# Kernel tuning notes

Measured on AMD Instinct MI355X. Metric: run time of the kernel, lower is better.

The kernel has to match this reference:

```python
import jax, jax.numpy as jnp
import numpy as np

B, N, DIM, H, DH, M, ROT = 2, 2048, 1024, 16, 64, 16, 32


def setup_inputs() -> dict:
    key = jax.random.key(0)
    ks = jax.random.split(key, 10)
    x = jax.random.normal(ks[0], (B, N, DIM), dtype=jnp.float32)
    # standard rotary frequency table, duplicated halves: [1,1,N,ROT]
    inv_freq = 1.0 / (10000.0 ** (jnp.arange(0, ROT, 2, dtype=jnp.float32) / ROT))
    t = jnp.arange(N, dtype=jnp.float32)
    fr = jnp.einsum('i,j->ij', t, inv_freq)
    rotary_pos_emb = jnp.concatenate([fr, fr], axis=-1)[None, None]
    s = 0.02
    Wq = jax.random.normal(ks[1], (H * DH, DIM), dtype=jnp.float32) * s
    Wk = jax.random.normal(ks[2], (H * DH, DIM), dtype=jnp.float32) * s
    Wv = jax.random.normal(ks[3], (H * DH, DIM), dtype=jnp.float32) * s
    mem_k = jax.random.normal(ks[4], (H, M, DH), dtype=jnp.float32)
    mem_v = jax.random.normal(ks[5], (H, M, DH), dtype=jnp.float32)
    pre_proj = jax.random.normal(ks[6], (H, H), dtype=jnp.float32)
    post_proj = jax.random.normal(ks[7], (H, H), dtype=jnp.float32)
    Wo = jax.random.normal(ks[8], (DIM, H * DH), dtype=jnp.float32) * s
    bo = jnp.zeros((DIM,), dtype=jnp.float32)
    return {'x': x, 'rotary_pos_emb': rotary_pos_emb, 'Wq': Wq, 'Wk': Wk, 'Wv': Wv,
            'mem_k': mem_k, 'mem_v': mem_v, 'pre_proj': pre_proj,
            'post_proj': post_proj, 'Wo': Wo, 'bo': bo}


def _rotate_half(t):
    d = t.shape[-1] // 2
    return jnp.concatenate([-t[..., d:], t[..., :d]], axis=-1)


def reference(x, rotary_pos_emb, Wq, Wk, Wv, mem_k, mem_v, pre_proj, post_proj, Wo, bo):
    b, n, _ = x.shape
    h, m, dh = mem_k.shape
    scale = dh ** -0.5
    # QKV projections -> [b, h, n, dh]
    q = (x @ Wq.T).reshape(b, n, h, dh).transpose(0, 2, 1, 3)
    k = (x @ Wk.T).reshape(b, n, h, dh).transpose(0, 2, 1, 3)
    v = (x @ Wv.T).reshape(b, n, h, dh).transpose(0, 2, 1, 3)
    # rotary on first l dims of q and k
    l = rotary_pos_emb.shape[-1]
    fr = rotary_pos_emb[:, :, -n:]  # [1,1,n,l]
    cos, sin = jnp.cos(fr), jnp.sin(fr)

    def apply_rot(t):
        tl, tr = t[..., :l], t[..., l:]
        return jnp.concatenate([tl * cos + _rotate_half(tl) * sin, tr], axis=-1)

    q, k = apply_rot(q), apply_rot(k)
    # memory key/values prepended on the key axis
    k = jnp.concatenate([jnp.broadcast_to(mem_k[None], (b, h, m, dh)), k], axis=2)
    v = jnp.concatenate([jnp.broadcast_to(mem_v[None], (b, h, m, dh)), v], axis=2)
    dots = jnp.einsum('bhid,bhjd->bhij', q, k) * scale
    pre_softmax_attn = dots
    # talking heads (pre-softmax head mixing)
    dots = jnp.einsum('bhij,hk->bkij', dots, pre_proj)
    # causal mask; first (j-i) memory columns always visible
    i, j = dots.shape[-2], dots.shape[-1]
    row = jnp.arange(i)[:, None]
    col = jnp.arange(j)[None, :]
    causal = (col - (j - i)) > row  # True where masked
    mask_value = -jnp.finfo(dots.dtype).max
    dots = jnp.where(causal, mask_value, dots)
    attn = jax.nn.softmax(dots, axis=-1)
    post_softmax_attn = attn
    # talking heads (post-softmax head mixing)
    attn = jnp.einsum('bhij,hk->bkij', attn, post_proj)
    out = jnp.einsum('bhij,bhjd->bhid', attn, v)
    out = out.transpose(0, 2, 1, 3).reshape(b, n, h * dh)
    out = out @ Wo.T + bo
    return (out, pre_softmax_attn, post_softmax_attn)
```

## Files before the change

kernel.cpp:

```cpp
#include <hip/hip_runtime.h>
#include <cstdint>
#include <cstddef>

#define HS_ ((size_t)2048 * 2064)

#define MIX16(D, sh, Prow) do { \
    const float4 _p0 = *(const float4*)&(Prow)[0]; \
    const float4 _p1 = *(const float4*)&(Prow)[4]; \
    const float4 _p2 = *(const float4*)&(Prow)[8]; \
    const float4 _p3 = *(const float4*)&(Prow)[12]; \
    D[0]  += (sh)*_p0.x; D[1]  += (sh)*_p0.y; D[2]  += (sh)*_p0.z; D[3]  += (sh)*_p0.w; \
    D[4]  += (sh)*_p1.x; D[5]  += (sh)*_p1.y; D[6]  += (sh)*_p1.z; D[7]  += (sh)*_p1.w; \
    D[8]  += (sh)*_p2.x; D[9]  += (sh)*_p2.y; D[10] += (sh)*_p2.z; D[11] += (sh)*_p2.w; \
    D[12] += (sh)*_p3.x; D[13] += (sh)*_p3.y; D[14] += (sh)*_p3.z; D[15] += (sh)*_p3.w; \
} while (0)

__global__ __launch_bounds__(256) void gemm128(const float* __restrict__ A,
    const float* __restrict__ B0, const float* __restrict__ B1, const float* __restrict__ B2,
    float* __restrict__ C, const float* __restrict__ bias, int ncols)
{
    __shared__ float As[16][132];
    __shared__ float Bs[16][132];
    const int tid = threadIdx.x;
    const int r0 = blockIdx.y * 128;
    const int xt = blockIdx.x;
    const float* Bm = (xt < 8) ? B0 : (xt < 16) ? B1 : B2;
    const int o_local  = (xt & 7) * 128;
    const int o_global = xt * 128;
    const int ty = tid >> 4, tx = tid & 15;
    float acc[8][8];
#pragma unroll
    for (int i = 0; i < 8; ++i)
#pragma unroll
        for (int j = 0; j < 8; ++j) acc[i][j] = 0.f;

    for (int k0 = 0; k0 < 1024; k0 += 16) {
        __syncthreads();
#pragma unroll
        for (int q = 0; q < 2; ++q) {
            const int f  = tid * 2 + q;
            const int rr = f >> 2;
            const int c4 = (f & 3) << 2;
            const float4 av = *(const float4*)(A  + (size_t)(r0 + rr)      * 1024 + k0 + c4);
            As[c4+0][rr] = av.x; As[c4+1][rr] = av.y; As[c4+2][rr] = av.z; As[c4+3][rr] = av.w;
            const float4 bv = *(const float4*)(Bm + (size_t)(o_local + rr) * 1024 + k0 + c4);
            Bs[c4+0][rr] = bv.x; Bs[c4+1][rr] = bv.y; Bs[c4+2][rr] = bv.z; Bs[c4+3][rr] = bv.w;
        }
        __syncthreads();
#pragma unroll
        for (int kk = 0; kk < 16; ++kk) {
            float a[8], bb[8];
            *(float4*)&a[0]  = *(const float4*)&As[kk][ty*8];
            *(float4*)&a[4]  = *(const float4*)&As[kk][ty*8+4];
            *(float4*)&bb[0] = *(const float4*)&Bs[kk][tx*8];
            *(float4*)&bb[4] = *(const float4*)&Bs[kk][tx*8+4];
#pragma unroll
            for (int i = 0; i < 8; ++i)
#pragma unroll
                for (int j = 0; j < 8; ++j) acc[i][j] += a[i] * bb[j];
        }
    }
#pragma unroll
    for (int i = 0; i < 8; ++i) {
        const int r = r0 + ty*8 + i;
        const int c = o_global + tx*8;
        float4 o0, o1;
        o0.x = acc[i][0]; o0.y = acc[i][1]; o0.z = acc[i][2]; o0.w = acc[i][3];
        o1.x = acc[i][4]; o1.y = acc[i][5]; o1.z = acc[i][6]; o1.w = acc[i][7];
        if (bias) {
            o0.x += bias[c+0]; o0.y += bias[c+1]; o0.z += bias[c+2]; o0.w += bias[c+3];
            o1.x += bias[c+4]; o1.y += bias[c+5]; o1.z += bias[c+6]; o1.w += bias[c+7];
        }
        *(float4*)(C + (size_t)r * ncols + c)     = o0;
        *(float4*)(C + (size_t)r * ncols + c + 4) = o1;
    }
}

__global__ __launch_bounds__(256) void rot_scatter(const float* __restrict__ qkv,
    const float* __restrict__ rope, float* __restrict__ q,
    float* __restrict__ kb, float* __restrict__ vb)
{
    __shared__ float cs_[32], sn_[32];
    const int r = blockIdx.x;
    const int m = blockIdx.y;
    const int b = r >> 11, n = r & 2047;
    if (threadIdx.x < 32) {
        const float fr = rope[n * 32 + threadIdx.x];
        cs_[threadIdx.x] = cosf(fr);
        sn_[threadIdx.x] = sinf(fr);
    }
    __syncthreads();
    const float* src = qkv + (size_t)r * 3072 + (size_t)m * 1024;
#pragma unroll
    for (int rep = 0; rep < 4; ++rep) {
        const int idx = rep * 256 + threadIdx.x;
        const int h = idx >> 6, d = idx & 63;
        float val = src[idx];
        if (m < 2 && d < 32) {
            const float p = src[(h << 6) | (d ^ 16)];
            val = val * cs_[d] + ((d < 16) ? -p : p) * sn_[d];
        }
        if (m == 0)      q [((size_t)(b*16 + h) * 2048 + n)      * 64 + d] = val;
        else if (m == 1) kb[((size_t)(b*16 + h) * 2064 + 16 + n) * 64 + d] = val;
        else             vb[((size_t)(b*16 + h) * 2064 + 16 + n) * 64 + d] = val;
    }
}

__global__ __launch_bounds__(256) void memfill(const float* __restrict__ mk,
    const float* __restrict__ mv, float* __restrict__ kb, float* __restrict__ vb)
{
    const int idx = blockIdx.x * 256 + threadIdx.x;
    if (idx >= 2*16*16*64) return;
    const int d  = idx & 63;
    const int mm = (idx >> 6) & 15;
    const int h  = (idx >> 10) & 15;
    const int b  = idx >> 14;
    const size_t dst = ((size_t)(b*16 + h) * 2064 + mm) * 64 + d;
    const size_t s   = (size_t)(h*16 + mm) * 64 + d;
    kb[dst] = mk[s];
    vb[dst] = mv[s];
}

__global__ __launch_bounds__(256) void qk_kernel(const float* __restrict__ q,
    const float* __restrict__ kb, float* __restrict__ S)
{
    __shared__ float Qs[64][68];
    __shared__ float Ks[64][68];
    const int tid = threadIdx.x;
    const int j0 = blockIdx.x * 64, i0 = blockIdx.y * 64, bh = blockIdx.z;
    const int rr = tid >> 2, qq = tid & 3;
    {
        const float4* qs = (const float4*)(q + ((size_t)bh * 2048 + i0 + rr) * 64 + qq * 16);
#pragma unroll
        for (int e = 0; e < 4; ++e) {
            const float4 t = qs[e]; const int c = qq*16 + e*4;
            Qs[c+0][rr] = t.x; Qs[c+1][rr] = t.y; Qs[c+2][rr] = t.z; Qs[c+3][rr] = t.w;
        }
        const int jrow = j0 + rr;
        if (jrow < 2064) {
            const float4* ks = (const float4*)(kb + ((size_t)bh * 2064 + jrow) * 64 + qq * 16);
#pragma unroll
            for (int e = 0; e < 4; ++e) {
                const float4 t = ks[e]; const int c = qq*16 + e*4;
                Ks[c+0][rr] = t.x; Ks[c+1][rr] = t.y; Ks[c+2][rr] = t.z; Ks[c+3][rr] = t.w;
            }
        } else {
#pragma unroll
            for (int e = 0; e < 16; ++e) Ks[qq*16 + e][rr] = 0.f;
        }
    }
    __syncthreads();
    const int ty = tid >> 4, tx = tid & 15;
    float acc[4][4];
#pragma unroll
    for (int i = 0; i < 4; ++i)
#pragma unroll
        for (int j = 0; j < 4; ++j) acc[i][j] = 0.f;
#pragma unroll
    for (int kk = 0; kk < 64; ++kk) {
        const float4 a4 = *(const float4*)&Qs[kk][ty * 4];
        const float4 b4 = *(const float4*)&Ks[kk][tx * 4];
        acc[0][0] += a4.x*b4.x; acc[0][1] += a4.x*b4.y; acc[0][2] += a4.x*b4.z; acc[0][3] += a4.x*b4.w;
        acc[1][0] += a4.y*b4.x; acc[1][1] += a4.y*b4.y; acc[1][2] += a4.y*b4.z; acc[1][3] += a4.y*b4.w;
        acc[2][0] += a4.z*b4.x; acc[2][1] += a4.z*b4.y; acc[2][2] += a4.z*b4.z; acc[2][3] += a4.z*b4.w;
        acc[3][0] += a4.w*b4.x; acc[3][1] += a4.w*b4.y; acc[3][2] += a4.w*b4.z; acc[3][3] += a4.w*b4.w;
    }
    const int jcol = j0 + tx*4;
    if (jcol < 2064) {
#pragma unroll
        for (int i = 0; i < 4; ++i) {
            float4 o4;
            o4.x = acc[i][0]*0.125f; o4.y = acc[i][1]*0.125f;
            o4.z = acc[i][2]*0.125f; o4.w = acc[i][3]*0.125f;
            *(float4*)(S + ((size_t)bh * 2048 + i0 + ty*4 + i) * 2064 + jcol) = o4;
        }
    }
}

__global__ __launch_bounds__(256) void stats_kernel(const float* __restrict__ S,
    const float* __restrict__ prew, float* __restrict__ mOut, float* __restrict__ lOut)
{
    __shared__ float P[16][20];
    __shared__ float red[4][16][2];
    const int tid = threadIdx.x;
    P[tid >> 4][tid & 15] = prew[tid];
    __syncthreads();
    const int bi = blockIdx.x;
    const int b = bi >> 11, i = bi & 2047;
    const float* Sb_ = S + (size_t)b * 16 * HS_ + (size_t)i * 2064;
    float m[16], l[16];
#pragma unroll
    for (int k = 0; k < 16; ++k) { m[k] = -3.0e38f; l[k] = 0.f; }
    const int jmax = i + 16;
    for (int jj = tid; jj <= jmax; jj += 256) {
        float D[16];
#pragma unroll
        for (int k = 0; k < 16; ++k) D[k] = 0.f;
#pragma unroll
        for (int h = 0; h < 16; ++h) {
            const float sh = Sb_[(size_t)h * HS_ + jj];
            MIX16(D, sh, P[h]);
        }
#pragma unroll
        for (int k = 0; k < 16; ++k) {
            const float dv = D[k];
            const float M  = fmaxf(m[k], dv);
            l[k] = l[k] * __expf(m[k] - M) + __expf(dv - M);
            m[k] = M;
        }
    }
#pragma unroll
    for (int off = 1; off < 64; off <<= 1) {
#pragma unroll
        for (int k = 0; k < 16; ++k) {
            const float mo = __shfl_xor(m[k], off);
            const float lo = __shfl_xor(l[k], off);
            const float M  = fmaxf(m[k], mo);
            l[k] = l[k] * __expf(m[k] - M) + lo * __expf(mo - M);
            m[k] = M;
        }
    }
    const int wv = tid >> 6, lane = tid & 63;
    if (lane == 0) {
#pragma unroll
        for (int k = 0; k < 16; ++k) { red[wv][k][0] = m[k]; red[wv][k][1] = l[k]; }
    }
    __syncthreads();
    if (tid < 16) {
        float M = red[0][tid][0], L = red[0][tid][1];
#pragma unroll
        for (int w = 1; w < 4; ++w) {
            const float mo = red[w][tid][0], lo = red[w][tid][1];
            const float Mn = fmaxf(M, mo);
            L = L * __expf(M - Mn) + lo * __expf(mo - Mn);
            M = Mn;
        }
        mOut[((size_t)b*16 + tid) * 2048 + i] = M;
        lOut[((size_t)b*16 + tid) * 2048 + i] = 1.0f / L;
    }
}

__global__ __launch_bounds__(256) void zerofill(float* __restrict__ post)
{
    const int row = blockIdx.x;
    const int i = row & 2047;
    float* p = post + (size_t)row * 2064;
    for (int j = i + 17 + threadIdx.x; j < 2064; j += 256) p[j] = 0.f;
}

__global__ __launch_bounds__(256) void fused_kernel(const float* __restrict__ S,
    float* __restrict__ Apost, const float* __restrict__ vb,
    const float* __restrict__ prew, const float* __restrict__ postw,
    const float* __restrict__ mIn, const float* __restrict__ lIn,
    float* __restrict__ ho)
{
    __shared__ float A2t[5184];
    __shared__ float Pp[16][20], Po[16][20];
    __shared__ float Ms[16][16], Ls[16][16];
    const int tid = threadIdx.x;
    const int it = blockIdx.x, jc = blockIdx.y, b = blockIdx.z;
    const int i0 = it * 16;
    const int tmax = it + 1;
    if (jc > tmax) return;
    {
        const int h = tid >> 4, c = tid & 15;
        Pp[h][c] = prew[tid];
        Po[h][c] = postw[tid];
        Ms[h][c] = mIn[((size_t)b*16 + h) * 2048 + i0 + c];
        Ls[h][c] = lIn[((size_t)b*16 + h) * 2048 + i0 + c];
    }
    __syncthreads();
    const int il = tid >> 4, jl = tid & 15;
    float msr[16], lsr[16];
#pragma unroll
    for (int k = 0; k < 16; ++k) { msr[k] = Ms[k][il]; lsr[k] = Ls[k][il]; }
    const int ig = i0 + il;
    const float* Sbase = S     + (size_t)b*16*HS_ + (size_t)ig * 2064 + jl;
    float*       Pbase = Apost + (size_t)b*16*HS_ + (size_t)ig * 2064 + jl;
    const int kh = il, dq = jl;
    const float* Vbase = vb + ((size_t)(b*16 + kh) * 2064) * 64 + dq * 4;
    float* a2w       = &A2t[jl*20 + il];
    const float* a2r = &A2t[kh*324];
    float acc[16][4];
#pragma unroll
    for (int i = 0; i < 16; ++i)
#pragma unroll
        for (int e = 0; e < 4; ++e) acc[i][e] = 0.f;

    for (int t = jc; t <= tmax; t += 4) {
        const int j0 = t * 16;
        const int jg = j0 + jl;
        float D[16];
#pragma unroll
        for (int k = 0; k < 16; ++k) D[k] = 0.f;
#pragma unroll
        for (int h = 0; h < 16; ++h) {
            const float sh = Sbase[(size_t)h * HS_ + j0];
            MIX16(D, sh, Pp[h]);
        }
        const bool masked = jg > ig + 16;
        float A[16];
#pragma unroll
        for (int k = 0; k < 16; ++k)
            A[k] = masked ? 0.f : __expf(D[k] - msr[k]) * lsr[k];
#pragma unroll
        for (int k = 0; k < 16; ++k)
            Pbase[(size_t)k * HS_ + j0] = A[k];
        float A2[16];
#pragma unroll
        for (int k = 0; k < 16; ++k) A2[k] = 0.f;
#pragma unroll
        for (int h = 0; h < 16; ++h) {
            const float ah = A[h];
            MIX16(A2, ah, Po[h]);
        }
#pragma unroll
        for (int k = 0; k < 16; ++k) a2w[k * 324] = A2[k];
        __syncthreads();
#pragma unroll
        for (int j = 0; j < 16; ++j) {
            const float4 v4 = *(const float4*)(Vbase + (size_t)(j0 + j) * 64);
            const float* ap = a2r + j * 20;
#pragma unroll
            for (int qq = 0; qq < 4; ++qq) {
                const float4 a4 = *(const float4*)(ap + qq * 4);
                acc[qq*4+0][0] += a4.x*v4.x; acc[qq*4+0][1] += a4.x*v4.y;
                acc[qq*4+0][2] += a4.x*v4.z; acc[qq*4+0][3] += a4.x*v4.w;
                acc[qq*4+1][0] += a4.y*v4.x; acc[qq*4+1][1] += a4.y*v4.y;
                acc[qq*4+1][2] += a4.y*v4.z; acc[qq*4+1][3] += a4.y*v4.w;
                acc[qq*4+2][0] += a4.z*v4.x; acc[qq*4+2][1] += a4.z*v4.y;
                acc[qq*4+2][2] += a4.z*v4.z; acc[qq*4+2][3] += a4.z*v4.w;
                acc[qq*4+3][0] += a4.w*v4.x; acc[qq*4+3][1] += a4.w*v4.y;
                acc[qq*4+3][2] += a4.w*v4.z; acc[qq*4+3][3] += a4.w*v4.w;
            }
        }
        __syncthreads();
    }
#pragma unroll
    for (int i = 0; i < 16; ++i) {
        float* dst = ho + ((size_t)(b*2048 + i0 + i)) * 1024 + kh*64 + dq*4;
        atomicAdd(dst+0, acc[i][0]);
        atomicAdd(dst+1, acc[i][1]);
        atomicAdd(dst+2, acc[i][2]);
        atomicAdd(dst+3, acc[i][3]);
    }
}

extern "C" void kernel_launch(void* const* d_in, const int* in_sizes, int n_in,
                              void* d_out, int out_size, void* d_ws, size_t ws_size,
                              hipStream_t stream)
{
    const float* x     = (const float*)d_in[0];
    const float* rope  = (const float*)d_in[1];
    const float* Wq    = (const float*)d_in[2];
    const float* Wk    = (const float*)d_in[3];
    const float* Wv    = (const float*)d_in[4];
    const float* memk  = (const float*)d_in[5];
    const float* memv  = (const float*)d_in[6];
    const float* prew  = (const float*)d_in[7];
    const float* postw = (const float*)d_in[8];
    const float* Wo    = (const float*)d_in[9];
    const float* bo    = (const float*)d_in[10];

    float* out  = (float*)d_out;
    float* pre  = out + (size_t)4194304;
    float* post = pre + (size_t)135266304;

    float* qkv_raw = post;
    float* qbuf    = post + 12582912;
    float* kbuf    = post + 16777216;

    float* vbuf = (float*)d_ws;
    float* ho   = vbuf + 4227072;
    float* mst  = ho + 4194304;
    float* linv = mst + 65536;
    if (ws_size < (size_t)8552448 * 4) return;

    gemm128<<<dim3(24, 32), 256, 0, stream>>>(x, Wq, Wk, Wv, qkv_raw, nullptr, 3072);
    rot_scatter<<<dim3(4096, 3), 256, 0, stream>>>(qkv_raw, rope, qbuf, kbuf, vbuf);
    memfill<<<dim3(128), 256, 0, stream>>>(memk, memv, kbuf, vbuf);
    qk_kernel<<<dim3(33, 32, 32), 256, 0, stream>>>(qbuf, kbuf, pre);
    stats_kernel<<<dim3(4096), 256, 0, stream>>>(pre, prew, mst, linv);
    zerofill<<<dim3(65536), 256, 0, stream>>>(post);
    hipMemsetAsync(ho, 0, (size_t)4194304 * 4, stream);
    fused_kernel<<<dim3(128, 4, 2), 256, 0, stream>>>(pre, post, vbuf, prew, postw, mst, linv, ho);
    gemm128<<<dim3(8, 32), 256, 0, stream>>>(ho, Wo, Wo, Wo, out, bo, 1024);
}
```

Measured before the change: 2.776 ms.

## Enlarge QK tile rows and rebalance fused softmax-PV kernel with paired row tiles

The QK kernel now computes 128x64 tiles with 8x4 per-thread accumulators, so each K tile is reused across twice as many query rows. The fused softmax/post-mix/PV kernel moves to 512 threads over 32-wide key chunks, and each block handles a row tile together with its mirror (it and 127-it) to even out causal-triangle work across blocks. These changes aim to cut redundant loads and load imbalance, at the cost of more registers per thread and clamped out-of-range key reads.

```diff
diff --git a/kernel.cpp b/kernel.cpp
--- a/kernel.cpp
+++ b/kernel.cpp
@@ -124,55 +124,62 @@
 __global__ __launch_bounds__(256) void qk_kernel(const float* __restrict__ q,
     const float* __restrict__ kb, float* __restrict__ S)
 {
-    __shared__ float Qs[64][68];
+    __shared__ float Qs[64][132];
     __shared__ float Ks[64][68];
     const int tid = threadIdx.x;
-    const int j0 = blockIdx.x * 64, i0 = blockIdx.y * 64, bh = blockIdx.z;
-    const int rr = tid >> 2, qq = tid & 3;
+    const int j0 = blockIdx.x * 64, i0 = blockIdx.y * 128, bh = blockIdx.z;
     {
-        const float4* qs = (const float4*)(q + ((size_t)bh * 2048 + i0 + rr) * 64 + qq * 16);
+        const float* Qg = q + ((size_t)bh * 2048 + i0) * 64;
+#pragma unroll
+        for (int e = 0; e < 8; ++e) {
+            const int idx = e * 256 + tid;
+            const int row = idx >> 4;
+            const int c4  = (idx & 15) << 2;
+            const float4 t = *(const float4*)(Qg + (size_t)row * 64 + c4);
+            Qs[c4+0][row] = t.x; Qs[c4+1][row] = t.y; Qs[c4+2][row] = t.z; Qs[c4+3][row] = t.w;
+        }
+        const float* Kg = kb + ((size_t)bh * 2064) * 64;
 #pragma unroll
         for (int e = 0; e < 4; ++e) {
-            const float4 t = qs[e]; const int c = qq*16 + e*4;
-            Qs[c+0][rr] = t.x; Qs[c+1][rr] = t.y; Qs[c+2][rr] = t.z; Qs[c+3][rr] = t.w;
-        }
-        const int jrow = j0 + rr;
-        if (jrow < 2064) {
-            const float4* ks = (const float4*)(kb + ((size_t)bh * 2064 + jrow) * 64 + qq * 16);
-#pragma unroll
-            for (int e = 0; e < 4; ++e) {
-                const float4 t = ks[e]; const int c = qq*16 + e*4;
-                Ks[c+0][rr] = t.x; Ks[c+1][rr] = t.y; Ks[c+2][rr] = t.z; Ks[c+3][rr] = t.w;
+            const int idx = e * 256 + tid;
+            const int row = idx >> 4;
+            const int c4  = (idx & 15) << 2;
+            const int jrow = j0 + row;
+            if (jrow < 2064) {
+                const float4 t = *(const float4*)(Kg + (size_t)jrow * 64 + c4);
+                Ks[c4+0][row] = t.x; Ks[c4+1][row] = t.y; Ks[c4+2][row] = t.z; Ks[c4+3][row] = t.w;
+            } else {
+                Ks[c4+0][row] = 0.f; Ks[c4+1][row] = 0.f; Ks[c4+2][row] = 0.f; Ks[c4+3][row] = 0.f;
             }
-        } else {
-#pragma unroll
-            for (int e = 0; e < 16; ++e) Ks[qq*16 + e][rr] = 0.f;
         }
     }
     __syncthreads();
     const int ty = tid >> 4, tx = tid & 15;
-    float acc[4][4];
-#pragma unroll
-    for (int i = 0; i < 4; ++i)
+    float acc[8][4];
+#pragma unroll
+    for (int i = 0; i < 8; ++i)
 #pragma unroll
         for (int j = 0; j < 4; ++j) acc[i][j] = 0.f;
 #pragma unroll
     for (int kk = 0; kk < 64; ++kk) {
-        const float4 a4 = *(const float4*)&Qs[kk][ty * 4];
-        const float4 b4 = *(const float4*)&Ks[kk][tx * 4];
-        acc[0][0] += a4.x*b4.x; acc[0][1] += a4.x*b4.y; acc[0][2] += a4.x*b4.z; acc[0][3] += a4.x*b4.w;
-        acc[1][0] += a4.y*b4.x; acc[1][1] += a4.y*b4.y; acc[1][2] += a4.y*b4.z; acc[1][3] += a4.y*b4.w;
-        acc[2][0] += a4.z*b4.x; acc[2][1] += a4.z*b4.y; acc[2][2] += a4.z*b4.z; acc[2][3] += a4.z*b4.w;
-        acc[3][0] += a4.w*b4.x; acc[3][1] += a4.w*b4.y; acc[3][2] += a4.w*b4.z; acc[3][3] += a4.w*b4.w;
+        float a[8];
+        *(float4*)&a[0] = *(const float4*)&Qs[kk][ty*8];
+        *(float4*)&a[4] = *(const float4*)&Qs[kk][ty*8+4];
+        const float4 b4 = *(const float4*)&Ks[kk][tx*4];
+#pragma unroll
+        for (int i = 0; i < 8; ++i) {
+            acc[i][0] += a[i]*b4.x; acc[i][1] += a[i]*b4.y;
+            acc[i][2] += a[i]*b4.z; acc[i][3] += a[i]*b4.w;
+        }
     }
     const int jcol = j0 + tx*4;
     if (jcol < 2064) {
 #pragma unroll
-        for (int i = 0; i < 4; ++i) {
+        for (int i = 0; i < 8; ++i) {
             float4 o4;
             o4.x = acc[i][0]*0.125f; o4.y = acc[i][1]*0.125f;
             o4.z = acc[i][2]*0.125f; o4.w = acc[i][3]*0.125f;
-            *(float4*)(S + ((size_t)bh * 2048 + i0 + ty*4 + i) * 2064 + jcol) = o4;
+            *(float4*)(S + ((size_t)bh * 2048 + i0 + ty*8 + i) * 2064 + jcol) = o4;
         }
     }
 }
@@ -248,101 +255,108 @@
     for (int j = i + 17 + threadIdx.x; j < 2064; j += 256) p[j] = 0.f;
 }
 
-__global__ __launch_bounds__(256) void fused_kernel(const float* __restrict__ S,
+#define JP 34
+#define KP 544
+__global__ __launch_bounds__(512) void fused_kernel(const float* __restrict__ S,
     float* __restrict__ Apost, const float* __restrict__ vb,
     const float* __restrict__ prew, const float* __restrict__ postw,
     const float* __restrict__ mIn, const float* __restrict__ lIn,
     float* __restrict__ ho)
 {
-    __shared__ float A2t[5184];
+    __shared__ float A2t[16 * KP / 16 * 16];
     __shared__ float Pp[16][20], Po[16][20];
     __shared__ float Ms[16][16], Ls[16][16];
     const int tid = threadIdx.x;
-    const int it = blockIdx.x, jc = blockIdx.y, b = blockIdx.z;
-    const int i0 = it * 16;
-    const int tmax = it + 1;
-    if (jc > tmax) return;
-    {
-        const int h = tid >> 4, c = tid & 15;
-        Pp[h][c] = prew[tid];
-        Po[h][c] = postw[tid];
-        Ms[h][c] = mIn[((size_t)b*16 + h) * 2048 + i0 + c];
-        Ls[h][c] = lIn[((size_t)b*16 + h) * 2048 + i0 + c];
-    }
-    __syncthreads();
-    const int il = tid >> 4, jl = tid & 15;
-    float msr[16], lsr[16];
-#pragma unroll
-    for (int k = 0; k < 16; ++k) { msr[k] = Ms[k][il]; lsr[k] = Ls[k][il]; }
-    const int ig = i0 + il;
-    const float* Sbase = S     + (size_t)b*16*HS_ + (size_t)ig * 2064 + jl;
-    float*       Pbase = Apost + (size_t)b*16*HS_ + (size_t)ig * 2064 + jl;
-    const int kh = il, dq = jl;
-    const float* Vbase = vb + ((size_t)(b*16 + kh) * 2064) * 64 + dq * 4;
-    float* a2w       = &A2t[jl*20 + il];
-    const float* a2r = &A2t[kh*324];
-    float acc[16][4];
-#pragma unroll
-    for (int i = 0; i < 16; ++i)
-#pragma unroll
-        for (int e = 0; e < 4; ++e) acc[i][e] = 0.f;
-
-    for (int t = jc; t <= tmax; t += 4) {
-        const int j0 = t * 16;
-        const int jg = j0 + jl;
-        float D[16];
-#pragma unroll
-        for (int k = 0; k < 16; ++k) D[k] = 0.f;
-#pragma unroll
-        for (int h = 0; h < 16; ++h) {
-            const float sh = Sbase[(size_t)h * HS_ + j0];
-            MIX16(D, sh, Pp[h]);
-        }
-        const bool masked = jg > ig + 16;
-        float A[16];
-#pragma unroll
-        for (int k = 0; k < 16; ++k)
-            A[k] = masked ? 0.f : __expf(D[k] - msr[k]) * lsr[k];
-#pragma unroll
-        for (int k = 0; k < 16; ++k)
-            Pbase[(size_t)k * HS_ + j0] = A[k];
-        float A2[16];
-#pragma unroll
-        for (int k = 0; k < 16; ++k) A2[k] = 0.f;
-#pragma unroll
-        for (int h = 0; h < 16; ++h) {
-            const float ah = A[h];
-            MIX16(A2, ah, Po[h]);
-        }
-#pragma unroll
-        for (int k = 0; k < 16; ++k) a2w[k * 324] = A2[k];
+    const int itp = blockIdx.x, jc = blockIdx.y, b = blockIdx.z;
+    if (tid < 256) {
+        Pp[tid >> 4][tid & 15] = prew[tid];
+        Po[tid >> 4][tid & 15] = postw[tid];
+    }
+    const int il = tid >> 5, jl = tid & 31;
+    const int kh = tid >> 5;
+    const int ih = (tid >> 4) & 1, dq = tid & 15;
+    const float* Vb0 = vb + ((size_t)(b*16 + kh) * 2064) * 64 + dq * 4;
+
+#pragma unroll 1
+    for (int seg = 0; seg < 2; ++seg) {
+        const int it = seg ? (127 - itp) : itp;
+        const int i0 = it * 16;
+        const int ig = i0 + il;
+        if (tid < 256) {
+            const int h = tid >> 4, c = tid & 15;
+            Ms[h][c] = mIn[((size_t)b*16 + h) * 2048 + i0 + c];
+            Ls[h][c] = lIn[((size_t)b*16 + h) * 2048 + i0 + c];
+        }
         __syncthreads();
-#pragma unroll
-        for (int j = 0; j < 16; ++j) {
-            const float4 v4 = *(const float4*)(Vbase + (size_t)(j0 + j) * 64);
-            const float* ap = a2r + j * 20;
-#pragma unroll
-            for (int qq = 0; qq < 4; ++qq) {
-                const float4 a4 = *(const float4*)(ap + qq * 4);
-                acc[qq*4+0][0] += a4.x*v4.x; acc[qq*4+0][1] += a4.x*v4.y;
-                acc[qq*4+0][2] += a4.x*v4.z; acc[qq*4+0][3] += a4.x*v4.w;
-                acc[qq*4+1][0] += a4.y*v4.x; acc[qq*4+1][1] += a4.y*v4.y;
-                acc[qq*4+1][2] += a4.y*v4.z; acc[qq*4+1][3] += a4.y*v4.w;
-                acc[qq*4+2][0] += a4.z*v4.x; acc[qq*4+2][1] += a4.z*v4.y;
-                acc[qq*4+2][2] += a4.z*v4.z; acc[qq*4+2][3] += a4.z*v4.w;
-                acc[qq*4+3][0] += a4.w*v4.x; acc[qq*4+3][1] += a4.w*v4.y;
-                acc[qq*4+3][2] += a4.w*v4.z; acc[qq*4+3][3] += a4.w*v4.w;
+        const float* Sb = S     + (size_t)b*16*HS_ + (size_t)ig * 2064;
+        float*       Pb = Apost + (size_t)b*16*HS_ + (size_t)ig * 2064;
+        float acc[8][4];
+#pragma unroll
+        for (int r = 0; r < 8; ++r)
+#pragma unroll
+            for (int e = 0; e < 4; ++e) acc[r][e] = 0.f;
+
+        const int U = (it + 3) >> 1;
+#pragma unroll 1
+        for (int u = jc; u < U; u += 4) {
+            const int j0 = u * 32;
+            const int jg = j0 + jl;
+            const int sjg = (jg < 2064) ? jg : 2063;
+            float s[16];
+#pragma unroll
+            for (int h = 0; h < 16; ++h) s[h] = Sb[(size_t)h * HS_ + sjg];
+            float D[16];
+#pragma unroll
+            for (int k = 0; k < 16; ++k) D[k] = 0.f;
+#pragma unroll
+            for (int h = 0; h < 16; ++h) MIX16(D, s[h], Pp[h]);
+            const bool live = (jg <= ig + 16);
+            float A[16];
+#pragma unroll
+            for (int k = 0; k < 16; ++k) {
+                const float e = __expf(D[k] - Ms[k][il]) * Ls[k][il];
+                A[k] = live ? e : 0.f;
             }
-        }
-        __syncthreads();
-    }
-#pragma unroll
-    for (int i = 0; i < 16; ++i) {
-        float* dst = ho + ((size_t)(b*2048 + i0 + i)) * 1024 + kh*64 + dq*4;
-        atomicAdd(dst+0, acc[i][0]);
-        atomicAdd(dst+1, acc[i][1]);
-        atomicAdd(dst+2, acc[i][2]);
-        atomicAdd(dst+3, acc[i][3]);
+            if (jg < 2064) {
+#pragma unroll
+                for (int k = 0; k < 16; ++k) Pb[(size_t)k * HS_ + jg] = A[k];
+            }
+            float A2[16];
+#pragma unroll
+            for (int k = 0; k < 16; ++k) A2[k] = 0.f;
+#pragma unroll
+            for (int h = 0; h < 16; ++h) MIX16(A2, A[h], Po[h]);
+            float* w = &A2t[il * JP + jl];
+#pragma unroll
+            for (int k = 0; k < 16; ++k) w[k * KP] = A2[k];
+            __syncthreads();
+            const float* ar = &A2t[kh * KP + (ih * 8) * JP];
+#pragma unroll
+            for (int j = 0; j < 32; j += 2) {
+                int ja0 = j0 + j, ja1 = j0 + j + 1;
+                ja0 = (ja0 < 2064) ? ja0 : 2063;
+                ja1 = (ja1 < 2064) ? ja1 : 2063;
+                const float4 va = *(const float4*)(Vb0 + (size_t)ja0 * 64);
+                const float4 vc = *(const float4*)(Vb0 + (size_t)ja1 * 64);
+#pragma unroll
+                for (int r = 0; r < 8; ++r) {
+                    const float2 a2 = *(const float2*)(ar + r * JP + j);
+                    acc[r][0] += a2.x * va.x + a2.y * vc.x;
+                    acc[r][1] += a2.x * va.y + a2.y * vc.y;
+                    acc[r][2] += a2.x * va.z + a2.y * vc.z;
+                    acc[r][3] += a2.x * va.w + a2.y * vc.w;
+                }
+            }
+            __syncthreads();
+        }
+#pragma unroll
+        for (int r = 0; r < 8; ++r) {
+            float* dst = ho + ((size_t)(b*2048 + i0 + ih*8 + r)) * 1024 + kh*64 + dq*4;
+            atomicAdd(dst+0, acc[r][0]);
+            atomicAdd(dst+1, acc[r][1]);
+            atomicAdd(dst+2, acc[r][2]);
+            atomicAdd(dst+3, acc[r][3]);
+        }
     }
 }
 
@@ -379,10 +393,10 @@
     gemm128<<<dim3(24, 32), 256, 0, stream>>>(x, Wq, Wk, Wv, qkv_raw, nullptr, 3072);
     rot_scatter<<<dim3(4096, 3), 256, 0, stream>>>(qkv_raw, rope, qbuf, kbuf, vbuf);
     memfill<<<dim3(128), 256, 0, stream>>>(memk, memv, kbuf, vbuf);
-    qk_kernel<<<dim3(33, 32, 32), 256, 0, stream>>>(qbuf, kbuf, pre);
+    qk_kernel<<<dim3(33, 16, 32), 256, 0, stream>>>(qbuf, kbuf, pre);
     stats_kernel<<<dim3(4096), 256, 0, stream>>>(pre, prew, mst, linv);
     zerofill<<<dim3(65536), 256, 0, stream>>>(post);
     hipMemsetAsync(ho, 0, (size_t)4194304 * 4, stream);
-    fused_kernel<<<dim3(128, 4, 2), 256, 0, stream>>>(pre, post, vbuf, prew, postw, mst, linv, ho);
+    fused_kernel<<<dim3(64, 4, 2), 512, 0, stream>>>(pre, post, vbuf, prew, postw, mst, linv, ho);
     gemm128<<<dim3(8, 32), 256, 0, stream>>>(ho, Wo, Wo, Wo, out, bo, 1024);
 }
```

New measurement: 2.537 ms. -8.6%, faster.
